# Performance work log

Measured on AMD Instinct MI355X. Metric: run time of the kernel, lower is better.

The kernel has to match this reference:

```python
import jax, jax.numpy as jnp
import numpy as np


def setup_inputs() -> dict:
    key = jax.random.key(0)
    k1, k2 = jax.random.split(key)
    x = jax.random.normal(k1, (32, 56, 56, 256), dtype=jnp.float32)
    conv_w = jax.random.normal(k2, (7, 7, 2, 1), dtype=jnp.float32) * 0.1
    conv_b = jnp.zeros((1,), dtype=jnp.float32)
    return {"x": x, "conv_w": conv_w, "conv_b": conv_b}


def reference(x, conv_w, conv_b):
    # x: [B, H, W, C] (NHWC, as in Keras)
    avg_pool = jnp.mean(x, axis=-1, keepdims=True)          # [B,H,W,1]
    max_pool = jnp.max(x, axis=-1, keepdims=True)           # [B,H,W,1]
    concat = jnp.concatenate([avg_pool, max_pool], axis=-1)  # [B,H,W,2]
    # 7x7 'same' conv, 2 -> 1 channels, HWIO kernel layout
    attn = jax.lax.conv_general_dilated(
        concat, conv_w,
        window_strides=(1, 1), padding='SAME',
        dimension_numbers=('NHWC', 'HWIO', 'NHWC'))
    attn = jax.nn.sigmoid(attn + conv_b)                     # [B,H,W,1]
    return x * attn
```

## Files before the change

### kernel.cpp

```cpp
#include <hip/hip_runtime.h>
#include <math.h>

#define BB 32
#define HH 56
#define WW 56
#define NPIX (BB * HH * WW)

typedef float vfloat4 __attribute__((ext_vector_type(4)));

#define POOL_BLOCKS 2048
#define POOL_WAVES (POOL_BLOCKS * 4)
__global__ __launch_bounds__(256) void pool_kernel(const float* __restrict__ x,
                                                   float* __restrict__ pooled) {
    const int wave = (blockIdx.x * 256 + threadIdx.x) >> 6;
    const int lane = threadIdx.x & 63;
    const vfloat4* x4 = (const vfloat4*)x;

    for (int pg = wave; pg < NPIX / 4; pg += POOL_WAVES) {
        const int p0 = pg * 4;
        float s[4], m[4];
#pragma unroll
        for (int j = 0; j < 4; ++j) {
            vfloat4 v = x4[(size_t)(p0 + j) * 64 + lane];
            s[j] = (v.x + v.y) + (v.z + v.w);
            m[j] = fmaxf(fmaxf(v.x, v.y), fmaxf(v.z, v.w));
        }
#pragma unroll
        for (int o = 32; o > 0; o >>= 1) {
#pragma unroll
            for (int j = 0; j < 4; ++j) {
                s[j] += __shfl_down(s[j], o, 64);
                m[j] = fmaxf(m[j], __shfl_down(m[j], o, 64));
            }
        }
        if (lane == 0) {
#pragma unroll
            for (int j = 0; j < 4; ++j) {
                pooled[(p0 + j) * 2]     = s[j] * (1.0f / 256.0f);
                pooled[(p0 + j) * 2 + 1] = m[j];
            }
        }
    }
}

__global__ __launch_bounds__(256) void conv_scale_kernel(
    const float* __restrict__ x,
    const float* __restrict__ pooled,
    const float* __restrict__ cw,
    const float* __restrict__ cb,
    float* __restrict__ out) {
    __shared__ float attn_s[64];
    const int pix0 = blockIdx.x * 64;
    const int t = threadIdx.x;

    if (t < 64) {
        const int idx = pix0 + t;
        const int b  = idx / (HH * WW);
        const int hw = idx % (HH * WW);
        const int h  = hw / WW;
        const int w  = hw % WW;
        float acc = cb[0];
        const float* base = pooled + (size_t)b * HH * WW * 2;
#pragma unroll
        for (int dh = 0; dh < 7; ++dh) {
            const int ih = h + dh - 3;
            if (ih < 0 || ih >= HH) continue;
#pragma unroll
            for (int dw = 0; dw < 7; ++dw) {
                const int iw = w + dw - 3;
                if (iw < 0 || iw >= WW) continue;
                const float* p = base + (ih * WW + iw) * 2;
                const float* k = cw + (dh * 7 + dw) * 2;
                acc = fmaf(p[0], k[0], acc);
                acc = fmaf(p[1], k[1], acc);
            }
        }
        attn_s[t] = 1.0f / (1.0f + expf(-acc));
    }
    __syncthreads();

    const int wv = t >> 6;
    const int lane = t & 63;
    const vfloat4* x4 = (const vfloat4*)x;
    vfloat4* o4 = (vfloat4*)out;
#pragma unroll 4
    for (int j = 0; j < 16; ++j) {
        const int p = wv * 16 + j;
        const size_t gi = (size_t)(pix0 + p) * 64 + lane;
        const float a = attn_s[p];
        vfloat4 v = x4[gi];
        v.x *= a; v.y *= a; v.z *= a; v.w *= a;
        __builtin_nontemporal_store(v, &o4[gi]);
    }
}

extern "C" void kernel_launch(void* const* d_in, const int* in_sizes, int n_in,
                              void* d_out, int out_size, void* d_ws, size_t ws_size,
                              hipStream_t stream) {
    const float* x  = (const float*)d_in[0];
    const float* cw = (const float*)d_in[1];
    const float* cb = (const float*)d_in[2];
    float* out = (float*)d_out;
    float* pooled = (float*)d_ws;

    pool_kernel<<<POOL_BLOCKS, 256, 0, stream>>>(x, pooled);
    conv_scale_kernel<<<NPIX / 64, 256, 0, stream>>>(x, pooled, cw, cb, out);
}
```

Before: 202.7 us.

## Fuse channel pooling, 7x7 conv and scaling into one tiled kernel

Replaces the separate pooling and conv/scale kernels with one kernel where each block owns a 4x14 spatial tile, recomputes mean/max pooling for its 10x20 halo into shared memory, runs the 7x7 conv and sigmoid from shared memory, then scales its own pixels. This drops the pooled workspace round trip and the second launch, and the scale pass should reread x mostly from cache. In exchange, halo pixels are pooled redundantly, about 3.5x the reads of x per tile, which relies on L2/infinity cache to absorb the overlap.

After: 207.7 us. 2.5% more time.

```diff
diff --git a/kernel.cpp b/kernel.cpp
--- a/kernel.cpp
+++ b/kernel.cpp
@@ -4,63 +4,75 @@
 #define BB 32
 #define HH 56
 #define WW 56
-#define NPIX (BB * HH * WW)
+#define IMG_PIX (HH * WW)
+#define TILE_H 4
+#define TILE_W 14
+#define HALO_H (TILE_H + 6)
+#define HALO_W (TILE_W + 6)
+#define NSLOT  (HALO_H * HALO_W)
+#define OWNED  (TILE_H * TILE_W)
+#define TILES_PER_IMG ((HH / TILE_H) * (WW / TILE_W))
+#define NBLK (BB * TILES_PER_IMG)
 
 typedef float vfloat4 __attribute__((ext_vector_type(4)));
 
-#define POOL_BLOCKS 2048
-#define POOL_WAVES (POOL_BLOCKS * 4)
-__global__ __launch_bounds__(256) void pool_kernel(const float* __restrict__ x,
-                                                   float* __restrict__ pooled) {
-    const int wave = (blockIdx.x * 256 + threadIdx.x) >> 6;
-    const int lane = threadIdx.x & 63;
+__global__ __launch_bounds__(256) void fused_kernel(
+    const float* __restrict__ x,
+    const float* __restrict__ cw,
+    const float* __restrict__ cb,
+    float* __restrict__ out) {
+    __shared__ float2 halo[NSLOT];
+    __shared__ float  attn_s[OWNED];
+
+    const int bi   = blockIdx.x;
+    const int b    = bi / TILES_PER_IMG;
+    const int tile = bi % TILES_PER_IMG;
+    const int h0   = (tile / (WW / TILE_W)) * TILE_H;
+    const int w0   = (tile % (WW / TILE_W)) * TILE_W;
+    const int t    = threadIdx.x;
+    const int wv   = t >> 6;
+    const int lane = t & 63;
+    const int g    = lane >> 3;
+    const int c    = lane & 7;
+
     const vfloat4* x4 = (const vfloat4*)x;
+    const size_t img_base = (size_t)b * IMG_PIX;
 
-    for (int pg = wave; pg < NPIX / 4; pg += POOL_WAVES) {
-        const int p0 = pg * 4;
-        float s[4], m[4];
 #pragma unroll
-        for (int j = 0; j < 4; ++j) {
-            vfloat4 v = x4[(size_t)(p0 + j) * 64 + lane];
-            s[j] = (v.x + v.y) + (v.z + v.w);
-            m[j] = fmaxf(fmaxf(v.x, v.y), fmaxf(v.z, v.w));
-        }
+    for (int it = 0; it < 7; ++it) {
+        const int k = it * 32 + wv * 8 + g;
+        if (k < NSLOT) {
+            const int lh = k / HALO_W, lw = k % HALO_W;
+            const int ih = h0 + lh - 3, iw = w0 + lw - 3;
+            if (ih >= 0 && ih < HH && iw >= 0 && iw < WW) {
+                const vfloat4* p4 = x4 + (img_base + ih * WW + iw) * 64 + c;
+                vfloat4 v[8];
 #pragma unroll
-        for (int o = 32; o > 0; o >>= 1) {
+                for (int j = 0; j < 8; ++j) v[j] = p4[j * 8];
+                vfloat4 sv = v[0], mv = v[0];
 #pragma unroll
-            for (int j = 0; j < 4; ++j) {
-                s[j] += __shfl_down(s[j], o, 64);
-                m[j] = fmaxf(m[j], __shfl_down(m[j], o, 64));
-            }
-        }
-        if (lane == 0) {
+                for (int j = 1; j < 8; ++j) {
+                    sv += v[j];
+                    mv.x = fmaxf(mv.x, v[j].x); mv.y = fmaxf(mv.y, v[j].y);
+                    mv.z = fmaxf(mv.z, v[j].z); mv.w = fmaxf(mv.w, v[j].w);
+                }
+                float s = (sv.x + sv.y) + (sv.z + sv.w);
+                float m = fmaxf(fmaxf(mv.x, mv.y), fmaxf(mv.z, mv.w));
 #pragma unroll
-            for (int j = 0; j < 4; ++j) {
-                pooled[(p0 + j) * 2]     = s[j] * (1.0f / 256.0f);
-                pooled[(p0 + j) * 2 + 1] = m[j];
+                for (int mask = 4; mask > 0; mask >>= 1) {
+                    s += __shfl_xor(s, mask, 64);
+                    m = fmaxf(m, __shfl_xor(m, mask, 64));
+                }
+                if (c == 0) halo[k] = make_float2(s * (1.0f / 256.0f), m);
             }
         }
     }
-}
+    __syncthreads();
 
-__global__ __launch_bounds__(256) void conv_scale_kernel(
-    const float* __restrict__ x,
-    const float* __restrict__ pooled,
-    const float* __restrict__ cw,
-    const float* __restrict__ cb,
-    float* __restrict__ out) {
-    __shared__ float attn_s[64];
-    const int pix0 = blockIdx.x * 64;
-    const int t = threadIdx.x;
-
-    if (t < 64) {
-        const int idx = pix0 + t;
-        const int b  = idx / (HH * WW);
-        const int hw = idx % (HH * WW);
-        const int h  = hw / WW;
-        const int w  = hw % WW;
+    if (t < OWNED) {
+        const int r  = t / TILE_W, cc = t % TILE_W;
+        const int h = h0 + r, w = w0 + cc;
         float acc = cb[0];
-        const float* base = pooled + (size_t)b * HH * WW * 2;
 #pragma unroll
         for (int dh = 0; dh < 7; ++dh) {
             const int ih = h + dh - 3;
@@ -69,28 +81,26 @@
             for (int dw = 0; dw < 7; ++dw) {
                 const int iw = w + dw - 3;
                 if (iw < 0 || iw >= WW) continue;
-                const float* p = base + (ih * WW + iw) * 2;
-                const float* k = cw + (dh * 7 + dw) * 2;
-                acc = fmaf(p[0], k[0], acc);
-                acc = fmaf(p[1], k[1], acc);
+                const float2 pv = halo[(r + dh) * HALO_W + (cc + dw)];
+                const float* kk = cw + (dh * 7 + dw) * 2;
+                acc = fmaf(pv.x, kk[0], fmaf(pv.y, kk[1], acc));
             }
         }
         attn_s[t] = 1.0f / (1.0f + expf(-acc));
     }
     __syncthreads();
 
-    const int wv = t >> 6;
-    const int lane = t & 63;
-    const vfloat4* x4 = (const vfloat4*)x;
-    vfloat4* o4 = (vfloat4*)out;
-#pragma unroll 4
-    for (int j = 0; j < 16; ++j) {
-        const int p = wv * 16 + j;
-        const size_t gi = (size_t)(pix0 + p) * 64 + lane;
-        const float a = attn_s[p];
-        vfloat4 v = x4[gi];
-        v.x *= a; v.y *= a; v.z *= a; v.w *= a;
-        __builtin_nontemporal_store(v, &o4[gi]);
+    {
+        const size_t rowbase = (img_base + (size_t)(h0 + wv) * WW + w0) * 64;
+        vfloat4* o4 = (vfloat4*)out;
+#pragma unroll
+        for (int j = 0; j < TILE_W; ++j) {
+            const float a = attn_s[wv * TILE_W + j];
+            const size_t gi = rowbase + j * 64 + lane;
+            vfloat4 v = x4[gi];
+            v.x *= a; v.y *= a; v.z *= a; v.w *= a;
+            __builtin_nontemporal_store(v, (vfloat4*)&o4[gi]);
+        }
     }
 }
 
@@ -101,8 +111,5 @@
     const float* cw = (const float*)d_in[1];
     const float* cb = (const float*)d_in[2];
     float* out = (float*)d_out;
-    float* pooled = (float*)d_ws;
-
-    pool_kernel<<<POOL_BLOCKS, 256, 0, stream>>>(x, pooled);
-    conv_scale_kernel<<<NPIX / 64, 256, 0, stream>>>(x, pooled, cw, cb, out);
+    fused_kernel<<<NBLK, 256, 0, stream>>>(x, cw, cb, out);
 }
```
